# Kernel optimization log

Hardware: AMD Instinct MI355X
Metric: run time of the kernel (lower is better)

The kernel has to match this reference:

```python
import jax, jax.numpy as jnp
import numpy as np

B, T, D_MODEL = 2, 2048, 2048
N_HEAD, N_KV, HD = 32, 8, 64


def _rope_tables(T, hd, base=10000.0):
    # standard rotary tables, (T, hd) with frequencies repeated over both halves
    inv_freq = 1.0 / (base ** (np.arange(0, hd // 2, dtype=np.float32) / (hd // 2)))
    t = np.arange(T, dtype=np.float32)
    freqs = np.outer(t, inv_freq)            # (T, hd/2)
    emb = np.concatenate([freqs, freqs], axis=-1)  # (T, hd)
    return jnp.asarray(np.cos(emb)), jnp.asarray(np.sin(emb))


def setup_inputs() -> dict:
    key = jax.random.key(0)
    ks = jax.random.split(key, 5)
    cos, sin = _rope_tables(T, HD)
    s = 0.02
    return {
        "x": jax.random.normal(ks[0], (B, T, D_MODEL), jnp.float32),
        "cos": cos,
        "sin": sin,
        "Wq": jax.random.normal(ks[1], (N_HEAD * HD, D_MODEL), jnp.float32) * s,
        "Wk": jax.random.normal(ks[2], (N_KV * HD, D_MODEL), jnp.float32) * s,
        "Wv": jax.random.normal(ks[3], (N_KV * HD, D_MODEL), jnp.float32) * s,
        "Wo": jax.random.normal(ks[4], (D_MODEL, N_HEAD * HD), jnp.float32) * s,
    }


def _apply_rope(x, cos, sin):
    # x: (B, H, T, D); cos/sin: (T, D)
    D = x.shape[-1]
    x1, x2 = x[..., : D // 2], x[..., D // 2 :]
    rot = jnp.concatenate([-x2, x1], axis=-1)
    c = cos[: x.shape[-2]][None, None]
    s = sin[: x.shape[-2]][None, None]
    return x * c + rot * s


def reference(x, cos, sin, Wq, Wk, Wv, Wo):
    Bv, Tv, _ = x.shape
    q = (x @ Wq.T).reshape(Bv, Tv, N_HEAD, HD).transpose(0, 2, 1, 3)  # (B,H,T,D)
    k = (x @ Wk.T).reshape(Bv, Tv, N_KV, HD).transpose(0, 2, 1, 3)    # (B,Hkv,T,D)
    v = (x @ Wv.T).reshape(Bv, Tv, N_KV, HD).transpose(0, 2, 1, 3)
    q = _apply_rope(q, cos, sin)
    k = _apply_rope(k, cos, sin)
    repeat = N_HEAD // N_KV
    if repeat > 1:
        k = jnp.repeat(k, repeat, axis=1)
        v = jnp.repeat(v, repeat, axis=1)
    scale = 1.0 / jnp.sqrt(jnp.float32(HD)).astype(x.dtype)
    scores = jnp.einsum("bhqd,bhkd->bhqk", q, k) * scale
    causal = jnp.tril(jnp.ones((Tv, Tv), dtype=bool))
    scores = jnp.where(causal[None, None], scores, jnp.finfo(scores.dtype).min)
    attn = jax.nn.softmax(scores, axis=-1)
    out = jnp.einsum("bhqk,bhkd->bhqd", attn, v)
    out = out.transpose(0, 2, 1, 3).reshape(Bv, Tv, N_HEAD * HD)
    return out @ Wo.T
```

## Files before the change

kernel.cpp:

```cpp
#include <hip/hip_runtime.h>
#include <stdint.h>

#define B_SZ 2
#define T_SEQ 2048
#define DM 2048
#define NH 32
#define NKV 8
#define HD 64
#define QKV_W 3072

typedef unsigned short u16;
typedef __bf16 bf16x8 __attribute__((ext_vector_type(8)));
typedef float floatx4 __attribute__((ext_vector_type(4)));

__device__ __forceinline__ float bf2f(u16 u) {
  union { unsigned u; float f; } v; v.u = ((unsigned)u) << 16; return v.f;
}
__device__ __forceinline__ u16 f2bf(float f) {
  union { float f; unsigned u; } v; v.f = f;
  unsigned r = v.u + 0x7fff + ((v.u >> 16) & 1);
  return (u16)(r >> 16);
}
__device__ __forceinline__ unsigned pk2bf(float hi, float lo) {
  return __builtin_amdgcn_perm(__float_as_uint(hi), __float_as_uint(lo), 0x07060302u);
}
__device__ __forceinline__ float fexp2(float x) {
#if __has_builtin(__builtin_amdgcn_exp2f)
  return __builtin_amdgcn_exp2f(x);
#else
  return exp2f(x);
#endif
}

__device__ __forceinline__ void gld_lds16(const void* g, void* l) {
  __builtin_amdgcn_global_load_lds(
      (const __attribute__((address_space(1))) unsigned int*)g,
      (__attribute__((address_space(3))) unsigned int*)l, 16, 0, 0);
}

__device__ __forceinline__ ushort4 cvt4(float4 v) {
  ushort4 o;
  o.x = f2bf(v.x); o.y = f2bf(v.y); o.z = f2bf(v.z); o.w = f2bf(v.w);
  return o;
}

__global__ __launch_bounds__(256) void conv_in_kernel(
    const float* __restrict__ x,  u16* __restrict__ xb,
    const float* __restrict__ Wq, const float* __restrict__ Wk,
    const float* __restrict__ Wv, u16* __restrict__ wqkvb)
{
  const int tid = threadIdx.x;
  if (blockIdx.x < 2048) {
    int i = blockIdx.x * 256 + tid;
    const int stride = 2048 * 256;
    for (; i < 2097152; i += stride)
      ((ushort4*)xb)[i] = cvt4(((const float4*)x)[i]);
  } else {
    int i = (blockIdx.x - 2048) * 256 + tid;
    const int stride = 1536 * 256;
    for (; i < 1572864; i += stride) {
      float4 v;
      if (i < 1048576)      v = ((const float4*)Wq)[i];
      else if (i < 1310720) v = ((const float4*)Wk)[i - 1048576];
      else                  v = ((const float4*)Wv)[i - 1310720];
      ((ushort4*)wqkvb)[i] = cvt4(v);
    }
  }
}

__global__ __launch_bounds__(256) void gemm_qkv_kernel(
    const u16* __restrict__ A, const u16* __restrict__ Bt,
    u16* __restrict__ C)
{
  __shared__ __align__(16) u16 sA[128 * 64];
  __shared__ __align__(16) u16 sB[128 * 64];

  const int L   = blockIdx.y * 24 + blockIdx.x;
  const int wid = (L % 8) * 96 + (L / 8);
  const int n0 = (wid % 24) * 128;
  const int m0 = (wid / 24) * 128;
  const int K = 2048;

  const int tid  = threadIdx.x;
  const int lane = tid & 63;
  const int w    = tid >> 6;
  const int wm = w >> 1, wn = w & 1;
  const int lm = lane & 15, lq = lane >> 4;

  floatx4 acc[4][4];
  #pragma unroll
  for (int i = 0; i < 4; i++)
    #pragma unroll
    for (int j = 0; j < 4; j++) { floatx4 z = {0.f,0.f,0.f,0.f}; acc[i][j] = z; }

  const int srow   = tid >> 3;
  const int schunk = (tid & 7) ^ (srow & 7);
  const u16* ApG = A  + (size_t)(m0 + srow) * K + schunk * 8;
  const u16* BpG = Bt + (size_t)(n0 + srow) * K + schunk * 8;
  u16* sAd = sA + tid * 8;
  u16* sBd = sB + tid * 8;

  const int sw  = lm & 7;
  const int rba = (wm * 64 + lm) * 64;
  const int rbb = (wn * 64 + lm) * 64;
  const int c0  = (lq ^ sw) * 8;
  const int c1  = ((4 + lq) ^ sw) * 8;

  for (int k0 = 0; k0 < K; k0 += 64) {
    #pragma unroll
    for (int p = 0; p < 4; p++) {
      gld_lds16(ApG + (size_t)p * 32 * K + k0, sAd + p * 2048);
      gld_lds16(BpG + (size_t)p * 32 * K + k0, sBd + p * 2048);
    }
    __syncthreads();

    #pragma unroll
    for (int kk = 0; kk < 2; kk++) {
      const int ck = kk ? c1 : c0;
      bf16x8 af[4], bfr[4];
      #pragma unroll
      for (int mi = 0; mi < 4; mi++)
        af[mi] = *(const bf16x8*)(sA + rba + mi * 1024 + ck);
      #pragma unroll
      for (int ni = 0; ni < 4; ni++)
        bfr[ni] = *(const bf16x8*)(sB + rbb + ni * 1024 + ck);

      #pragma unroll
      for (int mi = 0; mi < 4; mi++)
        #pragma unroll
        for (int ni = 0; ni < 4; ni++)
          acc[mi][ni] = __builtin_amdgcn_mfma_f32_16x16x32_bf16(
              af[mi], bfr[ni], acc[mi][ni], 0, 0, 0);
    }
    __syncthreads();
  }

  #pragma unroll
  for (int mi = 0; mi < 4; mi++)
    #pragma unroll
    for (int ni = 0; ni < 4; ni++)
      #pragma unroll
      for (int r = 0; r < 4; r++) {
        int row = m0 + wm*64 + mi*16 + lq*4 + r;
        int col = n0 + wn*64 + ni*16 + lm;
        C[(size_t)row * QKV_W + col] = f2bf(acc[mi][ni][r]);
      }
}

__global__ __launch_bounds__(256) void gemm_out_kernel(
    const u16* __restrict__ A, const u16* __restrict__ Bt,
    float* __restrict__ C)
{
  __shared__ __align__(16) u16 sA[128 * 64];
  __shared__ __align__(16) u16 sB[128 * 64];

  const int L   = blockIdx.y * 16 + blockIdx.x;
  const int wid = (L % 8) * 64 + (L / 8);
  const int n0 = (wid % 16) * 128;
  const int m0 = (wid / 16) * 128;
  const int K = 2048;

  const int tid  = threadIdx.x;
  const int lane = tid & 63;
  const int w    = tid >> 6;
  const int wm = w >> 1, wn = w & 1;
  const int lm = lane & 15, lq = lane >> 4;

  floatx4 acc[4][4];
  #pragma unroll
  for (int i = 0; i < 4; i++)
    #pragma unroll
    for (int j = 0; j < 4; j++) { floatx4 z = {0.f,0.f,0.f,0.f}; acc[i][j] = z; }

  const int srow   = tid >> 3;
  const int schunk = (tid & 7) ^ (srow & 7);
  const u16* ApG = A  + (size_t)(m0 + srow) * K + schunk * 8;
  const u16* BpG = Bt + (size_t)(n0 + srow) * K + schunk * 8;
  u16* sAd = sA + tid * 8;
  u16* sBd = sB + tid * 8;

  const int sw  = lm & 7;
  const int rba = (wm * 64 + lm) * 64;
  const int rbb = (wn * 64 + lm) * 64;
  const int c0  = (lq ^ sw) * 8;
  const int c1  = ((4 + lq) ^ sw) * 8;

  for (int k0 = 0; k0 < K; k0 += 64) {
    #pragma unroll
    for (int p = 0; p < 4; p++) {
      gld_lds16(ApG + (size_t)p * 32 * K + k0, sAd + p * 2048);
      gld_lds16(BpG + (size_t)p * 32 * K + k0, sBd + p * 2048);
    }
    __syncthreads();

    #pragma unroll
    for (int kk = 0; kk < 2; kk++) {
      const int ck = kk ? c1 : c0;
      bf16x8 af[4], bfr[4];
      #pragma unroll
      for (int mi = 0; mi < 4; mi++)
        af[mi] = *(const bf16x8*)(sA + rba + mi * 1024 + ck);
      #pragma unroll
      for (int ni = 0; ni < 4; ni++)
        bfr[ni] = *(const bf16x8*)(sB + rbb + ni * 1024 + ck);

      #pragma unroll
      for (int mi = 0; mi < 4; mi++)
        #pragma unroll
        for (int ni = 0; ni < 4; ni++)
          acc[mi][ni] = __builtin_amdgcn_mfma_f32_16x16x32_bf16(
              af[mi], bfr[ni], acc[mi][ni], 0, 0, 0);
    }
    __syncthreads();
  }

  #pragma unroll
  for (int mi = 0; mi < 4; mi++)
    #pragma unroll
    for (int ni = 0; ni < 4; ni++)
      #pragma unroll
      for (int r = 0; r < 4; r++) {
        int row = m0 + wm*64 + mi*16 + lq*4 + r;
        int col = n0 + wn*64 + ni*16 + lm;
        C[(size_t)row * DM + col] = acc[mi][ni][r];
      }
}

#define QSCALE 0.180336880f
__global__ __launch_bounds__(256) void prep_kernel(
    const u16* __restrict__ qkv, const float* __restrict__ cosf,
    const float* __restrict__ sinf, const float* __restrict__ Wo,
    u16* __restrict__ wob, u16* __restrict__ qb,
    u16* __restrict__ kb, u16* __restrict__ vbt)
{
  __shared__ u16 tile[64][66];
  const int tid = threadIdx.x;

  if (blockIdx.x < 1024) {
    int i = blockIdx.x * 256 + tid;
    const int stride = 1024 * 256;
    for (; i < 1048576; i += stride)
      ((ushort4*)wob)[i] = cvt4(((const float4*)Wo)[i]);
  } else if (blockIdx.x < 5120) {
    const int bt = blockIdx.x - 1024;
    const int b = bt / T_SEQ, t = bt % T_SEQ;
    const u16* row = qkv + (size_t)bt * QKV_W;

    #pragma unroll
    for (int i = 0; i < 4; i++) {
      int idx = i * 256 + tid;
      int h = idx >> 5, dp = idx & 31;
      float x1 = bf2f(row[h * 64 + dp]);
      float x2 = bf2f(row[h * 64 + dp + 32]);
      float c = cosf[t * 64 + dp];
      float s = sinf[t * 64 + dp];
      float o1 = (x1 * c - x2 * s) * QSCALE;
      float o2 = (x2 * c + x1 * s) * QSCALE;
      size_t base = ((size_t)(b * NH + h) * T_SEQ + t) * HD + dp;
      qb[base]      = f2bf(o1);
      qb[base + 32] = f2bf(o2);
    }
    {
      int idx = tid;
      int kvh = idx >> 5, dp = idx & 31;
      float x1 = bf2f(row[2048 + kvh * 64 + dp]);
      float x2 = bf2f(row[2048 + kvh * 64 + dp + 32]);
      float c = cosf[t * 64 + dp];
      float s = sinf[t * 64 + dp];
      size_t base = ((size_t)(b * NKV + kvh) * T_SEQ + t) * HD + dp;
      kb[base]      = f2bf(x1 * c - x2 * s);
      kb[base + 32] = f2bf(x2 * c + x1 * s);
    }
  } else {
    const int idx2 = blockIdx.x - 5120;
    const int t0  = (idx2 & 31) * 64;
    const int kvh = (idx2 >> 5) & 7;
    const int b   = idx2 >> 8;

    #pragma unroll
    for (int i = 0; i < 16; i++) {
      int idx = i * 256 + tid;
      int r = idx >> 6, c = idx & 63;
      tile[r][c] = qkv[(size_t)(b * T_SEQ + t0 + r) * QKV_W + 2560 + kvh * 64 + c];
    }
    __syncthreads();
    #pragma unroll
    for (int i = 0; i < 16; i++) {
      int idx = i * 256 + tid;
      int d = idx >> 6, c = idx & 63;
      vbt[((size_t)(b * NKV + kvh) * HD + d) * T_SEQ + t0 + c] = tile[c][d];
    }
  }
}

__global__ __launch_bounds__(256, 3) void attn_kernel(
    const u16* __restrict__ qb, const u16* __restrict__ kb,
    const u16* __restrict__ vbt, u16* __restrict__ attn)
{
  __shared__ __align__(16) u16 sK[2][64 * 64];
  __shared__ __align__(16) u16 sV[2][64 * 64];
  __shared__ __align__(16) u16 sP[4][16][72];
  __shared__ float sAl[4][16];

  const int tid  = threadIdx.x;
  const int lane = tid & 63;
  const int w    = tid >> 6;

  const int l  = blockIdx.x;
  const int qt = 63 - (l >> 4);
  const int kv = l & 7;
  const int b  = (l >> 3) & 1;
  const int h  = kv * 4 + w;
  const int ktmax = qt >> 1;
  const int moff  = 32 * (qt & 1);

  const int lm = lane & 15, lq = lane >> 4;
  const int sw = lm & 7;

  bf16x8 qf[2][2];
  {
    const u16* qhead = qb + ((size_t)(b * NH + h) * T_SEQ + qt * 32) * HD;
    #pragma unroll
    for (int nq = 0; nq < 2; nq++) {
      const u16* qrow = qhead + (size_t)(nq * 16 + lm) * HD + lq * 8;
      qf[nq][0] = *(const bf16x8*)(qrow);
      qf[nq][1] = *(const bf16x8*)(qrow + 32);
    }
  }

  floatx4 o_acc[2][4];
  #pragma unroll
  for (int i = 0; i < 2; i++)
    #pragma unroll
    for (int j = 0; j < 4; j++) { floatx4 z = {0.f,0.f,0.f,0.f}; o_acc[i][j] = z; }
  float m_run[2] = {-1e30f, -1e30f};
  float l_run[2] = {0.f, 0.f};

  const u16* kbase = kb  + (size_t)(b * NKV + kv) * T_SEQ * HD;
  const u16* vbase = vbt + (size_t)(b * NKV + kv) * HD * T_SEQ;

  const int p0row = tid >> 3,        p1row = (256 + tid) >> 3;
  const int p0ck  = (tid & 7) ^ (p0row & 7), p1ck = ((256 + tid) & 7) ^ (p1row & 7);
  const u16* kp0 = kbase + (size_t)p0row * HD + p0ck * 8;
  const u16* kp1 = kbase + (size_t)p1row * HD + p1ck * 8;
  const u16* vp0 = vbase + (size_t)p0row * T_SEQ + p0ck * 8;
  const u16* vp1 = vbase + (size_t)p1row * T_SEQ + p1ck * 8;
  const int d0 = tid * 16, d1 = (256 + tid) * 16;

  auto compute_tile = [&](const u16* sKc, const u16* sVc, const bool diag) {
    bf16x8 kf[4][2], vf[4][2];
    #pragma unroll
    for (int nt = 0; nt < 4; nt++) {
      kf[nt][0] = *(const bf16x8*)(sKc + (((nt*16 + lm) * 8 + (lq ^ sw)) << 3));
      kf[nt][1] = *(const bf16x8*)(sKc + (((nt*16 + lm) * 8 + ((4 + lq) ^ sw)) << 3));
      vf[nt][0] = *(const bf16x8*)(sVc + (((nt*16 + lm) * 8 + (lq ^ sw)) << 3));
      vf[nt][1] = *(const bf16x8*)(sVc + (((nt*16 + lm) * 8 + ((4 + lq) ^ sw)) << 3));
    }

    floatx4 s_acc[2][4];
    __builtin_amdgcn_s_setprio(1);
    #pragma unroll
    for (int nq = 0; nq < 2; nq++)
      #pragma unroll
      for (int nt = 0; nt < 4; nt++) {
        floatx4 z = {0.f,0.f,0.f,0.f};
        z = __builtin_amdgcn_mfma_f32_16x16x32_bf16(kf[nt][0], qf[nq][0], z, 0, 0, 0);
        z = __builtin_amdgcn_mfma_f32_16x16x32_bf16(kf[nt][1], qf[nq][1], z, 0, 0, 0);
        s_acc[nq][nt] = z;
      }
    __builtin_amdgcn_s_setprio(0);

    #pragma unroll
    for (int nq = 0; nq < 2; nq++) {
      if (diag) {
        #pragma unroll
        for (int nt = 0; nt < 4; nt++)
          #pragma unroll
          for (int r = 0; r < 4; r++)
            if (nt * 16 + lq * 4 + r > nq * 16 + lm + moff) s_acc[nq][nt][r] = -1e30f;
      }

      float mloc = s_acc[nq][0][0];
      #pragma unroll
      for (int nt = 0; nt < 4; nt++)
        #pragma unroll
        for (int r = 0; r < 4; r++) mloc = fmaxf(mloc, s_acc[nq][nt][r]);
      mloc = fmaxf(mloc, __shfl_xor(mloc, 16));
      mloc = fmaxf(mloc, __shfl_xor(mloc, 32));

      float mnew = m_run[nq];
      if (!__all(mloc - m_run[nq] <= 8.0f)) {
        mnew = fmaxf(m_run[nq], mloc);
        float al = fexp2(m_run[nq] - mnew);
        m_run[nq] = mnew;
        l_run[nq] *= al;
        if (lq == 0) sAl[w][lm] = al;
        floatx4 alv = *(const floatx4*)&sAl[w][lq * 4];
        #pragma unroll
        for (int nd = 0; nd < 4; nd++)
          #pragma unroll
          for (int r = 0; r < 4; r++)
            o_acc[nq][nd][r] *= alv[r];
      }

      float rs = 0.f;
      uint2 pk[4];
      #pragma unroll
      for (int nt = 0; nt < 4; nt++) {
        float p0 = fexp2(s_acc[nq][nt][0] - mnew);
        float p1 = fexp2(s_acc[nq][nt][1] - mnew);
        float p2 = fexp2(s_acc[nq][nt][2] - mnew);
        float p3 = fexp2(s_acc[nq][nt][3] - mnew);
        rs += (p0 + p1) + (p2 + p3);
        pk[nt].x = pk2bf(p1, p0);
        pk[nt].y = pk2bf(p3, p2);
      }
      rs += __shfl_xor(rs, 16);
      rs += __shfl_xor(rs, 32);
      l_run[nq] += rs;

      #pragma unroll
      for (int nt = 0; nt < 4; nt++)
        *(uint2*)&sP[w][lm][nt * 16 + lq * 4] = pk[nt];

      __builtin_amdgcn_s_setprio(1);
      #pragma unroll
      for (int st = 0; st < 2; st++) {
        bf16x8 pf = *(const bf16x8*)(&sP[w][lm][st * 32 + lq * 8]);
        #pragma unroll
        for (int nd = 0; nd < 4; nd++)
          o_acc[nq][nd] = __builtin_amdgcn_mfma_f32_16x16x32_bf16(
              pf, vf[nd][st], o_acc[nq][nd], 0, 0, 0);
      }
      __builtin_amdgcn_s_setprio(0);
    }
  };

  const int nst = (ktmax >> 1) + 1;
  for (int s2 = 0; s2 < nst; s2++) {
    const int kt0  = s2 * 2;
    const int kt1  = kt0 + 1;
    const int kt1c = kt1 < 32 ? kt1 : 31;
    __syncthreads();
    gld_lds16(kp0 + (size_t)kt0  * 64 * HD, (char*)sK[0] + d0);
    gld_lds16(kp1 + (size_t)kt0  * 64 * HD, (char*)sK[0] + d1);
    gld_lds16(kp0 + (size_t)kt1c * 64 * HD, (char*)sK[1] + d0);
    gld_lds16(kp1 + (size_t)kt1c * 64 * HD, (char*)sK[1] + d1);
    gld_lds16(vp0 + kt0  * 64, (char*)sV[0] + d0);
    gld_lds16(vp1 + kt0  * 64, (char*)sV[0] + d1);
    gld_lds16(vp0 + kt1c * 64, (char*)sV[1] + d0);
    gld_lds16(vp1 + kt1c * 64, (char*)sV[1] + d1);
    __syncthreads();

    compute_tile(sK[0], sV[0], kt0 == ktmax);
    if (kt1 <= ktmax) compute_tile(sK[1], sV[1], kt1 == ktmax);
  }

  #pragma unroll
  for (int nq = 0; nq < 2; nq++) {
    __builtin_amdgcn_s_waitcnt(0);
    if (lq == 0) sAl[w][lm] = l_run[nq];
    floatx4 lv = *(const floatx4*)&sAl[w][lq * 4];
    #pragma unroll
    for (int nd = 0; nd < 4; nd++)
      #pragma unroll
      for (int r = 0; r < 4; r++) {
        float v = o_acc[nq][nd][r] / lv[r];
        size_t row = (size_t)b * T_SEQ + qt * 32 + nq * 16 + lq * 4 + r;
        attn[row * DM + h * HD + nd * 16 + lm] = f2bf(v);
      }
  }
}

extern "C" void kernel_launch(void* const* d_in, const int* in_sizes, int n_in,
                              void* d_out, int out_size, void* d_ws, size_t ws_size,
                              hipStream_t stream)
{
  const float* x    = (const float*)d_in[0];
  const float* cosf = (const float*)d_in[1];
  const float* sinf = (const float*)d_in[2];
  const float* Wq   = (const float*)d_in[3];
  const float* Wk   = (const float*)d_in[4];
  const float* Wv   = (const float*)d_in[5];
  const float* Wo   = (const float*)d_in[6];
  float* out = (float*)d_out;

  char* ws = (char*)d_ws;
  u16* qkvb  = (u16*)(ws + 0);
  u16* attnb = (u16*)(ws + 0);
  u16* qb    = (u16*)(ws + 25165824);
  u16* kb    = (u16*)(ws + 41943040);
  u16* vbt   = (u16*)(ws + 46137344);
  u16* xb    = (u16*)(ws + 50331648);
  u16* wob   = (u16*)(ws + 50331648);
  u16* wqkvb = (u16*)(ws + 67108864);

  dim3 blk(256);
  conv_in_kernel<<<dim3(3584), blk, 0, stream>>>(x, xb, Wq, Wk, Wv, wqkvb);

  gemm_qkv_kernel<<<dim3(24, 32), blk, 0, stream>>>(xb, wqkvb, qkvb);

  prep_kernel<<<dim3(5632), blk, 0, stream>>>(qkvb, cosf, sinf, Wo, wob,
                                              qb, kb, vbt);
  attn_kernel<<<dim3(1024), blk, 0, stream>>>(qb, kb, vbt, attnb);
  gemm_out_kernel<<<dim3(16, 32), blk, 0, stream>>>(attnb, wob, out);
}
```

Measured before the change: 279.4 us.

## Halve attention query tile to 16 rows and single-buffer K/V per tile

```diff
diff --git a/kernel.cpp b/kernel.cpp
--- a/kernel.cpp
+++ b/kernel.cpp
@@ -293,12 +293,12 @@
   }
 }
 
-__global__ __launch_bounds__(256, 3) void attn_kernel(
+__global__ __launch_bounds__(256, 4) void attn_kernel(
     const u16* __restrict__ qb, const u16* __restrict__ kb,
     const u16* __restrict__ vbt, u16* __restrict__ attn)
 {
-  __shared__ __align__(16) u16 sK[2][64 * 64];
-  __shared__ __align__(16) u16 sV[2][64 * 64];
+  __shared__ __align__(16) u16 sK[64 * 64];
+  __shared__ __align__(16) u16 sV[64 * 64];
   __shared__ __align__(16) u16 sP[4][16][72];
   __shared__ float sAl[4][16];
 
@@ -307,34 +307,28 @@
   const int w    = tid >> 6;
 
   const int l  = blockIdx.x;
-  const int qt = 63 - (l >> 4);
+  const int qt = 127 - (l >> 4);
   const int kv = l & 7;
   const int b  = (l >> 3) & 1;
   const int h  = kv * 4 + w;
-  const int ktmax = qt >> 1;
-  const int moff  = 32 * (qt & 1);
+  const int ktmax = qt >> 2;
+  const int moff  = 16 * (qt & 3);
 
   const int lm = lane & 15, lq = lane >> 4;
   const int sw = lm & 7;
 
-  bf16x8 qf[2][2];
+  bf16x8 qf[2];
   {
-    const u16* qhead = qb + ((size_t)(b * NH + h) * T_SEQ + qt * 32) * HD;
-    #pragma unroll
-    for (int nq = 0; nq < 2; nq++) {
-      const u16* qrow = qhead + (size_t)(nq * 16 + lm) * HD + lq * 8;
-      qf[nq][0] = *(const bf16x8*)(qrow);
-      qf[nq][1] = *(const bf16x8*)(qrow + 32);
-    }
-  }
-
-  floatx4 o_acc[2][4];
-  #pragma unroll
-  for (int i = 0; i < 2; i++)
-    #pragma unroll
-    for (int j = 0; j < 4; j++) { floatx4 z = {0.f,0.f,0.f,0.f}; o_acc[i][j] = z; }
-  float m_run[2] = {-1e30f, -1e30f};
-  float l_run[2] = {0.f, 0.f};
+    const u16* qrow = qb + ((size_t)(b * NH + h) * T_SEQ + qt * 16 + lm) * HD + lq * 8;
+    qf[0] = *(const bf16x8*)(qrow);
+    qf[1] = *(const bf16x8*)(qrow + 32);
+  }
+
+  floatx4 o_acc[4];
+  #pragma unroll
+  for (int j = 0; j < 4; j++) { floatx4 z = {0.f,0.f,0.f,0.f}; o_acc[j] = z; }
+  float m_run = -1e30f;
+  float l_run = 0.f;
 
   const u16* kbase = kb  + (size_t)(b * NKV + kv) * T_SEQ * HD;
   const u16* vbase = vbt + (size_t)(b * NKV + kv) * HD * T_SEQ;
@@ -345,131 +339,111 @@
   const u16* kp1 = kbase + (size_t)p1row * HD + p1ck * 8;
   const u16* vp0 = vbase + (size_t)p0row * T_SEQ + p0ck * 8;
   const u16* vp1 = vbase + (size_t)p1row * T_SEQ + p1ck * 8;
-  const int d0 = tid * 16, d1 = (256 + tid) * 16;
-
-  auto compute_tile = [&](const u16* sKc, const u16* sVc, const bool diag) {
+  char* sKd0 = (char*)sK + tid * 16;        char* sKd1 = (char*)sK + (256 + tid) * 16;
+  char* sVd0 = (char*)sV + tid * 16;        char* sVd1 = (char*)sV + (256 + tid) * 16;
+
+  for (int kt = 0; kt <= ktmax; kt++) {
+    __syncthreads();
+    gld_lds16(kp0 + (size_t)kt * 64 * HD, sKd0);
+    gld_lds16(kp1 + (size_t)kt * 64 * HD, sKd1);
+    gld_lds16(vp0 + kt * 64, sVd0);
+    gld_lds16(vp1 + kt * 64, sVd1);
+    __syncthreads();
+
     bf16x8 kf[4][2], vf[4][2];
     #pragma unroll
     for (int nt = 0; nt < 4; nt++) {
-      kf[nt][0] = *(const bf16x8*)(sKc + (((nt*16 + lm) * 8 + (lq ^ sw)) << 3));
-      kf[nt][1] = *(const bf16x8*)(sKc + (((nt*16 + lm) * 8 + ((4 + lq) ^ sw)) << 3));
-      vf[nt][0] = *(const bf16x8*)(sVc + (((nt*16 + lm) * 8 + (lq ^ sw)) << 3));
-      vf[nt][1] = *(const bf16x8*)(sVc + (((nt*16 + lm) * 8 + ((4 + lq) ^ sw)) << 3));
-    }
-
-    floatx4 s_acc[2][4];
+      kf[nt][0] = *(const bf16x8*)(sK + (((nt*16 + lm) * 8 + (lq ^ sw)) << 3));
+      kf[nt][1] = *(const bf16x8*)(sK + (((nt*16 + lm) * 8 + ((4 + lq) ^ sw)) << 3));
+      vf[nt][0] = *(const bf16x8*)(sV + (((nt*16 + lm) * 8 + (lq ^ sw)) << 3));
+      vf[nt][1] = *(const bf16x8*)(sV + (((nt*16 + lm) * 8 + ((4 + lq) ^ sw)) << 3));
+    }
+
+    floatx4 s_acc[4];
     __builtin_amdgcn_s_setprio(1);
     #pragma unroll
-    for (int nq = 0; nq < 2; nq++)
-      #pragma unroll
-      for (int nt = 0; nt < 4; nt++) {
-        floatx4 z = {0.f,0.f,0.f,0.f};
-        z = __builtin_amdgcn_mfma_f32_16x16x32_bf16(kf[nt][0], qf[nq][0], z, 0, 0, 0);
-        z = __builtin_amdgcn_mfma_f32_16x16x32_bf16(kf[nt][1], qf[nq][1], z, 0, 0, 0);
-        s_acc[nq][nt] = z;
-      }
+    for (int nt = 0; nt < 4; nt++) {
+      floatx4 z = {0.f,0.f,0.f,0.f};
+      z = __builtin_amdgcn_mfma_f32_16x16x32_bf16(kf[nt][0], qf[0], z, 0, 0, 0);
+      z = __builtin_amdgcn_mfma_f32_16x16x32_bf16(kf[nt][1], qf[1], z, 0, 0, 0);
+      s_acc[nt] = z;
+    }
     __builtin_amdgcn_s_setprio(0);
 
-    #pragma unroll
-    for (int nq = 0; nq < 2; nq++) {
-      if (diag) {
-        #pragma unroll
-        for (int nt = 0; nt < 4; nt++)
-          #pragma unroll
-          for (int r = 0; r < 4; r++)
-            if (nt * 16 + lq * 4 + r > nq * 16 + lm + moff) s_acc[nq][nt][r] = -1e30f;
-      }
-
-      float mloc = s_acc[nq][0][0];
+    if (kt == ktmax) {
       #pragma unroll
       for (int nt = 0; nt < 4; nt++)
         #pragma unroll
-        for (int r = 0; r < 4; r++) mloc = fmaxf(mloc, s_acc[nq][nt][r]);
-      mloc = fmaxf(mloc, __shfl_xor(mloc, 16));
-      mloc = fmaxf(mloc, __shfl_xor(mloc, 32));
-
-      float mnew = m_run[nq];
-      if (!__all(mloc - m_run[nq] <= 8.0f)) {
-        mnew = fmaxf(m_run[nq], mloc);
-        float al = fexp2(m_run[nq] - mnew);
-        m_run[nq] = mnew;
-        l_run[nq] *= al;
-        if (lq == 0) sAl[w][lm] = al;
-        floatx4 alv = *(const floatx4*)&sAl[w][lq * 4];
+        for (int r = 0; r < 4; r++)
+          if (nt * 16 + lq * 4 + r > lm + moff) s_acc[nt][r] = -1e30f;
+    }
+
+    float mloc = s_acc[0][0];
+    #pragma unroll
+    for (int nt = 0; nt < 4; nt++)
+      #pragma unroll
+      for (int r = 0; r < 4; r++) mloc = fmaxf(mloc, s_acc[nt][r]);
+    mloc = fmaxf(mloc, __shfl_xor(mloc, 16));
+    mloc = fmaxf(mloc, __shfl_xor(mloc, 32));
+
+    float mnew = m_run;
+    if (!__all(mloc - m_run <= 8.0f)) {
+      mnew = fmaxf(m_run, mloc);
+      float al = fexp2(m_run - mnew);
+      m_run = mnew;
+      l_run *= al;
+      if (lq == 0) sAl[w][lm] = al;
+      floatx4 alv = *(const floatx4*)&sAl[w][lq * 4];
+      #pragma unroll
+      for (int nd = 0; nd < 4; nd++)
         #pragma unroll
-        for (int nd = 0; nd < 4; nd++)
-          #pragma unroll
-          for (int r = 0; r < 4; r++)
-            o_acc[nq][nd][r] *= alv[r];
-      }
-
-      float rs = 0.f;
-      uint2 pk[4];
-      #pragma unroll
-      for (int nt = 0; nt < 4; nt++) {
-        float p0 = fexp2(s_acc[nq][nt][0] - mnew);
-        float p1 = fexp2(s_acc[nq][nt][1] - mnew);
-        float p2 = fexp2(s_acc[nq][nt][2] - mnew);
-        float p3 = fexp2(s_acc[nq][nt][3] - mnew);
-        rs += (p0 + p1) + (p2 + p3);
-        pk[nt].x = pk2bf(p1, p0);
-        pk[nt].y = pk2bf(p3, p2);
-      }
-      rs += __shfl_xor(rs, 16);
-      rs += __shfl_xor(rs, 32);
-      l_run[nq] += rs;
-
-      #pragma unroll
-      for (int nt = 0; nt < 4; nt++)
-        *(uint2*)&sP[w][lm][nt * 16 + lq * 4] = pk[nt];
-
-      __builtin_amdgcn_s_setprio(1);
-      #pragma unroll
-      for (int st = 0; st < 2; st++) {
-        bf16x8 pf = *(const bf16x8*)(&sP[w][lm][st * 32 + lq * 8]);
-        #pragma unroll
-        for (int nd = 0; nd < 4; nd++)
-          o_acc[nq][nd] = __builtin_amdgcn_mfma_f32_16x16x32_bf16(
-              pf, vf[nd][st], o_acc[nq][nd], 0, 0, 0);
-      }
-      __builtin_amdgcn_s_setprio(0);
-    }
-  };
-
-  const int nst = (ktmax >> 1) + 1;
-  for (int s2 = 0; s2 < nst; s2++) {
-    const int kt0  = s2 * 2;
-    const int kt1  = kt0 + 1;
-    const int kt1c = kt1 < 32 ? kt1 : 31;
-    __syncthreads();
-    gld_lds16(kp0 + (size_t)kt0  * 64 * HD, (char*)sK[0] + d0);
-    gld_lds16(kp1 + (size_t)kt0  * 64 * HD, (char*)sK[0] + d1);
-    gld_lds16(kp0 + (size_t)kt1c * 64 * HD, (char*)sK[1] + d0);
-    gld_lds16(kp1 + (size_t)kt1c * 64 * HD, (char*)sK[1] + d1);
-    gld_lds16(vp0 + kt0  * 64, (char*)sV[0] + d0);
-    gld_lds16(vp1 + kt0  * 64, (char*)sV[0] + d1);
-    gld_lds16(vp0 + kt1c * 64, (char*)sV[1] + d0);
-    gld_lds16(vp1 + kt1c * 64, (char*)sV[1] + d1);
-    __syncthreads();
-
-    compute_tile(sK[0], sV[0], kt0 == ktmax);
-    if (kt1 <= ktmax) compute_tile(sK[1], sV[1], kt1 == ktmax);
-  }
-
-  #pragma unroll
-  for (int nq = 0; nq < 2; nq++) {
-    __builtin_amdgcn_s_waitcnt(0);
-    if (lq == 0) sAl[w][lm] = l_run[nq];
-    floatx4 lv = *(const floatx4*)&sAl[w][lq * 4];
-    #pragma unroll
-    for (int nd = 0; nd < 4; nd++)
-      #pragma unroll
-      for (int r = 0; r < 4; r++) {
-        float v = o_acc[nq][nd][r] / lv[r];
-        size_t row = (size_t)b * T_SEQ + qt * 32 + nq * 16 + lq * 4 + r;
-        attn[row * DM + h * HD + nd * 16 + lm] = f2bf(v);
-      }
-  }
+        for (int r = 0; r < 4; r++)
+          o_acc[nd][r] *= alv[r];
+    }
+
+    float rs = 0.f;
+    uint2 pk[4];
+    #pragma unroll
+    for (int nt = 0; nt < 4; nt++) {
+      float p0 = fexp2(s_acc[nt][0] - mnew);
+      float p1 = fexp2(s_acc[nt][1] - mnew);
+      float p2 = fexp2(s_acc[nt][2] - mnew);
+      float p3 = fexp2(s_acc[nt][3] - mnew);
+      rs += (p0 + p1) + (p2 + p3);
+      pk[nt].x = pk2bf(p1, p0);
+      pk[nt].y = pk2bf(p3, p2);
+    }
+    rs += __shfl_xor(rs, 16);
+    rs += __shfl_xor(rs, 32);
+    l_run += rs;
+
+    #pragma unroll
+    for (int nt = 0; nt < 4; nt++)
+      *(uint2*)&sP[w][lm][nt * 16 + lq * 4] = pk[nt];
+
+    __builtin_amdgcn_s_setprio(1);
+    #pragma unroll
+    for (int st = 0; st < 2; st++) {
+      bf16x8 pf = *(const bf16x8*)(&sP[w][lm][st * 32 + lq * 8]);
+      #pragma unroll
+      for (int nd = 0; nd < 4; nd++)
+        o_acc[nd] = __builtin_amdgcn_mfma_f32_16x16x32_bf16(
+            pf, vf[nd][st], o_acc[nd], 0, 0, 0);
+    }
+    __builtin_amdgcn_s_setprio(0);
+  }
+
+  __builtin_amdgcn_s_waitcnt(0);
+  if (lq == 0) sAl[w][lm] = l_run;
+  floatx4 lv = *(const floatx4*)&sAl[w][lq * 4];
+  #pragma unroll
+  for (int nd = 0; nd < 4; nd++)
+    #pragma unroll
+    for (int r = 0; r < 4; r++) {
+      float v = o_acc[nd][r] / lv[r];
+      size_t row = (size_t)b * T_SEQ + qt * 16 + lq * 4 + r;
+      attn[row * DM + h * HD + nd * 16 + lm] = f2bf(v);
+    }
 }
 
 extern "C" void kernel_launch(void* const* d_in, const int* in_sizes, int n_in,
@@ -502,6 +476,6 @@
 
   prep_kernel<<<dim3(5632), blk, 0, stream>>>(qkvb, cosf, sinf, Wo, wob,
                                               qb, kb, vbt);
-  attn_kernel<<<dim3(1024), blk, 0, stream>>>(qb, kb, vbt, attnb);
+  attn_kernel<<<dim3(2048), blk, 0, stream>>>(qb, kb, vbt, attnb);
   gemm_out_kernel<<<dim3(16, 32), blk, 0, stream>>>(attnb, wob, out);
 }
```

New measurement: 284.6 us. Within noise of the previous version (+1.8%).
